# Kernel tuning notes

Measured on AMD Instinct MI355X. Metric: run time of the kernel, lower is better.

## Reference

```python
import jax, jax.numpy as jnp
import numpy as np

B, E, S = 8, 128, 4096


def setup_inputs() -> dict:
    key = jax.random.key(0)
    ks = jax.random.split(key, 7)
    sc = 1.0 / np.sqrt(E)
    return {
        "x": jax.random.normal(ks[0], (B, E, S), dtype=jnp.float32),
        "Wq": jax.random.normal(ks[1], (E, E), dtype=jnp.float32) * sc,
        "bq": jax.random.normal(ks[2], (E,), dtype=jnp.float32) * 0.01,
        "Wk": jax.random.normal(ks[3], (E, E), dtype=jnp.float32) * sc,
        "bk": jax.random.normal(ks[4], (E,), dtype=jnp.float32) * 0.01,
        "Wv": jax.random.normal(ks[5], (E, E), dtype=jnp.float32) * sc,
        "bv": jax.random.normal(ks[6], (E,), dtype=jnp.float32) * 0.01,
    }


def reference(x, Wq, bq, Wk, bk, Wv, bv):
    # x: [B, E, S]; Conv1d(k=1) == per-position linear over channels.
    # Project then move to [B, S, E] (matches .permute(0, 2, 1)).
    Q = jnp.einsum('bes,fe->bsf', x, Wq) + bq  # [B, S, E]
    K = jnp.einsum('bes,fe->bsf', x, Wk) + bk
    V = jnp.einsum('bes,fe->bsf', x, Wv) + bv
    scale = jnp.sqrt(jnp.asarray(float(x.shape[1]), dtype=jnp.float32))
    attn = jnp.einsum('bqe,bke->bqk', Q, K) / scale  # [B, S, S]
    attn = jax.nn.softmax(attn, axis=2)
    out = jnp.einsum('bqk,bke->bqe', attn, V)  # [B, S, E]
    return out.transpose(0, 2, 1)  # [B, E, S]
```

## Files before the change

kernel.cpp:

```cpp
#include <hip/hip_runtime.h>
#include <math.h>

#define NB 8
#define NE 128
#define NS 4096
#define CSCALE 0.12751743f

typedef short s8v __attribute__((ext_vector_type(8)));
typedef float f4v __attribute__((ext_vector_type(4)));
typedef float f16v __attribute__((ext_vector_type(16)));
typedef unsigned int u32;
typedef unsigned int u2v __attribute__((ext_vector_type(2)));
typedef __attribute__((address_space(1))) const u32* gp1_t;
typedef __attribute__((address_space(3))) u32* lp3_t;

__device__ __forceinline__ ushort f2bf(float f) {
  union { float f; unsigned u; } v; v.f = f;
  unsigned r = v.u + 0x7fffu + ((v.u >> 16) & 1u);
  return (ushort)(r >> 16);
}
__device__ __forceinline__ float bf2f(ushort h) {
  union { unsigned u; float f; } v; v.u = ((unsigned)h) << 16; return v.f;
}
__device__ __forceinline__ void gload_lds16(const void* g, void* l) {
  __builtin_amdgcn_global_load_lds((gp1_t)g, (lp3_t)l, 16, 0, 0);
}
__device__ __forceinline__ u32 cvtpk(float lo, float hi) {
  u32 r;
  asm("v_cvt_pk_bf16_f32 %0, %1, %2" : "=v"(r) : "v"(lo), "v"(hi));
  return r;
}
__device__ __forceinline__ void split8(const float* __restrict__ p, float scale,
                                       s8v& hi, s8v& lo) {
  union { s8v v; ushort u[8]; } H, L;
  #pragma unroll
  for (int i = 0; i < 8; ++i) {
    float v = p[i] * scale;
    ushort h = f2bf(v);
    H.u[i] = h;
    L.u[i] = f2bf(v - bf2f(h));
  }
  hi = H.v; lo = L.v;
}

__global__ __launch_bounds__(256, 2) void proj_gemm(
    const float* __restrict__ x,
    const float* __restrict__ Wq, const float* __restrict__ bq,
    const float* __restrict__ Wk, const float* __restrict__ bk,
    const float* __restrict__ Wv, const float* __restrict__ bv,
    ushort* __restrict__ Qn, ushort* __restrict__ Kn, ushort* __restrict__ Vt)
{
  const int tid = threadIdx.x;
  const int wv = tid >> 6, lane = tid & 63;
  const int g = lane >> 4, c = lane & 15;
  const int bid = blockIdx.x;
  const int b = bid & 7;
  const int s0 = (bid >> 3) * 64;
  const float* xb = x + (size_t)b * NE * NS;

  __shared__ __align__(16) ushort xh[64][136], xl[64][136];

  {
    const int ss = tid & 63, cq = tid >> 6;
    #pragma unroll
    for (int p = 0; p < 4; ++p) {
      const int ch = p * 4 + cq;
      union { s8v v; ushort u[8]; } H, L;
      #pragma unroll
      for (int i = 0; i < 8; ++i) {
        float v = xb[(size_t)(ch * 8 + i) * NS + s0 + ss];
        ushort hi = f2bf(v);
        H.u[i] = hi;
        L.u[i] = f2bf(v - bf2f(hi));
      }
      *(s8v*)&xh[ss][ch * 8] = H.v;
      *(s8v*)&xl[ss][ch * 8] = L.v;
    }
  }
  __syncthreads();

  f4v aq[2][4], ak[2][4], av[2][4];
  #pragma unroll
  for (int i = 0; i < 2; ++i)
    #pragma unroll
    for (int j = 0; j < 4; ++j) {
      aq[i][j] = (f4v){0.f,0.f,0.f,0.f};
      ak[i][j] = (f4v){0.f,0.f,0.f,0.f};
      av[i][j] = (f4v){0.f,0.f,0.f,0.f};
    }

  #pragma unroll
  for (int ks = 0; ks < 4; ++ks) {
    s8v xbh[4], xbl[4];
    #pragma unroll
    for (int st = 0; st < 4; ++st) {
      xbh[st] = *(const s8v*)&xh[st * 16 + c][ks * 32 + g * 8];
      xbl[st] = *(const s8v*)&xl[st * 16 + c][ks * 32 + g * 8];
    }
    #pragma unroll
    for (int ftl = 0; ftl < 2; ++ftl) {
      const int f0 = (wv * 2 + ftl) * 16;
      const size_t wo = (size_t)(f0 + c) * NE + ks * 32 + g * 8;
      s8v qh, ql, kh, kl, vh, vl;
      split8(Wq + wo, CSCALE, qh, ql);
      split8(Wk + wo, 1.0f,   kh, kl);
      split8(Wv + wo, 1.0f,   vh, vl);
      #pragma unroll
      for (int st = 0; st < 4; ++st) {
        aq[ftl][st] = __builtin_amdgcn_mfma_f32_16x16x32_bf16(xbh[st], qh, aq[ftl][st], 0, 0, 0);
        aq[ftl][st] = __builtin_amdgcn_mfma_f32_16x16x32_bf16(xbl[st], qh, aq[ftl][st], 0, 0, 0);
        aq[ftl][st] = __builtin_amdgcn_mfma_f32_16x16x32_bf16(xbh[st], ql, aq[ftl][st], 0, 0, 0);
        av[ftl][st] = __builtin_amdgcn_mfma_f32_16x16x32_bf16(vh, xbh[st], av[ftl][st], 0, 0, 0);
        av[ftl][st] = __builtin_amdgcn_mfma_f32_16x16x32_bf16(vh, xbl[st], av[ftl][st], 0, 0, 0);
        av[ftl][st] = __builtin_amdgcn_mfma_f32_16x16x32_bf16(vl, xbh[st], av[ftl][st], 0, 0, 0);
        ak[ftl][st] = __builtin_amdgcn_mfma_f32_16x16x32_bf16(xbh[st], kh, ak[ftl][st], 0, 0, 0);
        ak[ftl][st] = __builtin_amdgcn_mfma_f32_16x16x32_bf16(xbl[st], kh, ak[ftl][st], 0, 0, 0);
        ak[ftl][st] = __builtin_amdgcn_mfma_f32_16x16x32_bf16(xbh[st], kl, ak[ftl][st], 0, 0, 0);
      }
    }
  }

  ushort* Qnb = Qn + (size_t)b * NS * NE;
  ushort* Knb = Kn + (size_t)b * NS * NE;
  ushort* Vtb = Vt + (size_t)b * NE * NS;
  #pragma unroll
  for (int ftl = 0; ftl < 2; ++ftl) {
    const int f0 = (wv * 2 + ftl) * 16;
    #pragma unroll
    for (int r = 0; r < 4; ++r) {
      const int f = f0 + 4 * g + r;
      const float bvv = bv[f];
      #pragma unroll
      for (int st = 0; st < 4; ++st)
        Vtb[(size_t)f * NS + s0 + st * 16 + c] = f2bf(av[ftl][st][r] + bvv);
    }
    const float bqv = bq[f0 + c] * CSCALE;
    const float bkv = bk[f0 + c];
    #pragma unroll
    for (int st = 0; st < 4; ++st)
      #pragma unroll
      for (int r = 0; r < 4; ++r) {
        const size_t ro = (size_t)(s0 + st * 16 + 4 * g + r) * NE + f0 + c;
        Qnb[ro] = f2bf(aq[ftl][st][r] + bqv);
        Knb[ro] = f2bf(ak[ftl][st][r] + bkv);
      }
  }
}

__global__ __launch_bounds__(512, 2) void attn_kernel(
    const ushort* __restrict__ Qn, const ushort* __restrict__ Kn,
    const ushort* __restrict__ Vt, float* __restrict__ out)
{
  const int tid = threadIdx.x;
  const int w = tid >> 6, lane = tid & 63;
  const int h = lane >> 5, q5 = lane & 31;
  const int slice = w >> 2;
  const int sub = w & 3;
  const int bid = blockIdx.x;
  const int b = bid & 7;
  const int qw = (bid >> 3) * 128 + sub * 32;

  const ushort* Qb = Qn + (size_t)b * NS * NE;
  const char*   Kb = (const char*)(Kn + (size_t)b * NS * NE);
  const char*   Vb = (const char*)(Vt + (size_t)b * NE * NS);

  __shared__ __align__(16) char lds[131072];
  __shared__ float lx[2][4][32];

  auto Kbuf = [&](int bf) -> char* { return lds + slice * 65536 + bf * 32768; };
  auto Vbuf = [&](int bf) -> char* { return Kbuf(bf) + 16384; };

  s8v qf[8];
  #pragma unroll
  for (int dc = 0; dc < 8; ++dc)
    qf[dc] = *(const s8v*)(Qb + (size_t)(qw + q5) * NE + dc * 16 + h * 8);

  auto stage = [&](int bf, int t) {
    const int kt = slice * 32 + t;
    if (sub < 2) {
      const char* Ksrc = Kb + (size_t)kt * (64 * 256);
      char* dst = Kbuf(bf);
      const int base = sub * 8192;
      #pragma unroll
      for (int p = 0; p < 8; ++p) {
        const int off = base + p * 1024;
        const int lo = off + lane * 16;
        const int row = lo >> 8;
        gload_lds16(Ksrc + (lo ^ ((row & 15) << 4)), dst + off);
      }
    } else {
      char* dst = Vbuf(bf);
      const int base = (sub - 2) * 8192;
      #pragma unroll
      for (int p = 0; p < 8; ++p) {
        const int off = base + p * 1024;
        const int lo = off + lane * 16;
        const int row = lo >> 7;
        const int inner = (lo & 127) ^ ((row & 7) << 4);
        gload_lds16(Vb + (size_t)row * (NS * 2) + kt * 128 + inner, dst + off);
      }
    }
  };

  auto expfrag8 = [&](float a0, float a1, float a2, float a3,
                      float a4, float a5, float a6, float a7, float& l) -> s8v {
    float p0 = __builtin_amdgcn_exp2f(a0), p1 = __builtin_amdgcn_exp2f(a1);
    float p2 = __builtin_amdgcn_exp2f(a2), p3 = __builtin_amdgcn_exp2f(a3);
    float p4 = __builtin_amdgcn_exp2f(a4), p5 = __builtin_amdgcn_exp2f(a5);
    float p6 = __builtin_amdgcn_exp2f(a6), p7 = __builtin_amdgcn_exp2f(a7);
    l += ((p0 + p1) + (p2 + p3)) + ((p4 + p5) + (p6 + p7));
    u32 A = cvtpk(p0, p1);
    u32 B = cvtpk(p4, p5);
    u32 C = cvtpk(p2, p3);
    u32 D = cvtpk(p6, p7);
    u2v rAB = __builtin_amdgcn_permlane32_swap(A, B, false, false);
    u2v rCD = __builtin_amdgcn_permlane32_swap(C, D, false, false);
    union { s8v v; u32 wd[4]; } P;
    P.wd[0] = rAB[0]; P.wd[1] = rCD[0]; P.wd[2] = rAB[1]; P.wd[3] = rCD[1];
    return P.v;
  };

  f16v o[4];
  #pragma unroll
  for (int dt = 0; dt < 4; ++dt)
    o[dt] = (f16v){0,0,0,0,0,0,0,0,0,0,0,0,0,0,0,0};
  float lsum = 0.f;

  stage(0, 0);
  asm volatile("s_waitcnt vmcnt(0)" ::: "memory");
  __builtin_amdgcn_sched_barrier(0);
  __builtin_amdgcn_s_barrier();

  #pragma unroll 1
  for (int t = 0; t < 32; ++t) {
    const int cur = t & 1;
    if (t + 1 < 32) stage(cur ^ 1, t + 1);
    const char* bK = Kbuf(cur);
    const char* bV = Vbuf(cur);

    f16v s0 = (f16v){0,0,0,0,0,0,0,0,0,0,0,0,0,0,0,0};
    f16v s1 = (f16v){0,0,0,0,0,0,0,0,0,0,0,0,0,0,0,0};
    __builtin_amdgcn_s_setprio(1);
    #pragma unroll
    for (int dc = 0; dc < 8; ++dc) {
      s8v kf0 = *(const s8v*)(bK + (q5) * 256      + ((dc * 32 + h * 16) ^ ((q5 & 15) << 4)));
      s8v kf1 = *(const s8v*)(bK + (32 + q5) * 256 + ((dc * 32 + h * 16) ^ ((q5 & 15) << 4)));
      s0 = __builtin_amdgcn_mfma_f32_32x32x16_bf16(kf0, qf[dc], s0, 0, 0, 0);
      s1 = __builtin_amdgcn_mfma_f32_32x32x16_bf16(kf1, qf[dc], s1, 0, 0, 0);
    }
    __builtin_amdgcn_s_setprio(0);

    #pragma unroll
    for (int ks = 0; ks < 4; ++ks) {
      s8v P;
      if (ks == 0)      P = expfrag8(s0[0], s0[1], s0[2], s0[3], s0[4], s0[5], s0[6], s0[7], lsum);
      else if (ks == 1) P = expfrag8(s0[8], s0[9], s0[10], s0[11], s0[12], s0[13], s0[14], s0[15], lsum);
      else if (ks == 2) P = expfrag8(s1[0], s1[1], s1[2], s1[3], s1[4], s1[5], s1[6], s1[7], lsum);
      else              P = expfrag8(s1[8], s1[9], s1[10], s1[11], s1[12], s1[13], s1[14], s1[15], lsum);
      __builtin_amdgcn_s_setprio(1);
      #pragma unroll
      for (int dt = 0; dt < 4; ++dt) {
        s8v vf = *(const s8v*)(bV + (dt * 32 + q5) * 128 +
                               ((ks * 32 + h * 16) ^ ((q5 & 7) << 4)));
        o[dt] = __builtin_amdgcn_mfma_f32_32x32x16_bf16(vf, P, o[dt], 0, 0, 0);
      }
      __builtin_amdgcn_s_setprio(0);
    }

    asm volatile("s_waitcnt lgkmcnt(0)" ::: "memory");
    __builtin_amdgcn_sched_barrier(0);
    asm volatile("s_waitcnt vmcnt(0)" ::: "memory");
    __builtin_amdgcn_sched_barrier(0);
    __builtin_amdgcn_s_barrier();
  }

  lsum += __shfl_xor(lsum, 32);
  if (h == 0) lx[slice][sub][q5] = lsum;
  float* cb = (float*)lds;
  __syncthreads();
  if (slice == 1) {
    #pragma unroll
    for (int dt = 0; dt < 4; ++dt)
      #pragma unroll
      for (int r = 0; r < 16; ++r) {
        const int e = dt * 32 + (r & 3) + 8 * (r >> 2) + 4 * h;
        cb[sub * 4096 + e * 32 + q5] = o[dt][r];
      }
  }
  __syncthreads();
  if (slice == 0) {
    const float rinv = 1.0f / (lx[0][sub][q5] + lx[1][sub][q5]);
    float* ob = out + (size_t)b * NE * NS;
    #pragma unroll
    for (int dt = 0; dt < 4; ++dt)
      #pragma unroll
      for (int r = 0; r < 16; ++r) {
        const int e = dt * 32 + (r & 3) + 8 * (r >> 2) + 4 * h;
        ob[(size_t)e * NS + qw + q5] =
            (o[dt][r] + cb[sub * 4096 + e * 32 + q5]) * rinv;
      }
  }
}

extern "C" void kernel_launch(void* const* d_in, const int* in_sizes, int n_in,
                              void* d_out, int out_size, void* d_ws, size_t ws_size,
                              hipStream_t stream) {
  (void)in_sizes; (void)n_in; (void)out_size; (void)ws_size;
  const float* x  = (const float*)d_in[0];
  const float* Wq = (const float*)d_in[1];
  const float* bq = (const float*)d_in[2];
  const float* Wk = (const float*)d_in[3];
  const float* bk = (const float*)d_in[4];
  const float* Wv = (const float*)d_in[5];
  const float* bv = (const float*)d_in[6];
  float* out = (float*)d_out;

  ushort* Qn = (ushort*)d_ws;
  ushort* Kn = Qn + (size_t)NB * NS * NE;
  ushort* Vt = Kn + (size_t)NB * NS * NE;

  proj_gemm<<<dim3(NS / 64 * NB), 256, 0, stream>>>(x, Wq, bq, Wk, bk, Wv, bv, Qn, Kn, Vt);
  attn_kernel<<<dim3(NS / 128 * NB), 512, 0, stream>>>(Qn, Kn, Vt, out);
}
```

Before: 101.9 us.

## Software-pipeline QK and PV across tiles with lagged V staging

Measured after the change: 100.7 us. No clear change (-1.2%).

```diff
diff --git a/kernel.cpp b/kernel.cpp
--- a/kernel.cpp
+++ b/kernel.cpp
@@ -175,9 +175,9 @@
   for (int dc = 0; dc < 8; ++dc)
     qf[dc] = *(const s8v*)(Qb + (size_t)(qw + q5) * NE + dc * 16 + h * 8);
 
-  auto stage = [&](int bf, int t) {
-    const int kt = slice * 32 + t;
+  auto stageK = [&](int bf, int t) {
     if (sub < 2) {
+      const int kt = slice * 32 + t;
       const char* Ksrc = Kb + (size_t)kt * (64 * 256);
       char* dst = Kbuf(bf);
       const int base = sub * 8192;
@@ -188,16 +188,21 @@
         const int row = lo >> 8;
         gload_lds16(Ksrc + (lo ^ ((row & 15) << 4)), dst + off);
       }
-    } else {
+    }
+  };
+  auto stageV = [&](int bf, int t) {
+    if (sub >= 2) {
+      const int kt = slice * 32 + t;
       char* dst = Vbuf(bf);
       const int base = (sub - 2) * 8192;
       #pragma unroll
       for (int p = 0; p < 8; ++p) {
         const int off = base + p * 1024;
         const int lo = off + lane * 16;
-        const int row = lo >> 7;
-        const int inner = (lo & 127) ^ ((row & 7) << 4);
-        gload_lds16(Vb + (size_t)row * (NS * 2) + kt * 128 + inner, dst + off);
+        const int row = lo >> 8;
+        const int inner = (lo & 255) ^ ((row & 15) << 4);
+        const int d = row + (inner >> 7) * 64;
+        gload_lds16(Vb + (size_t)d * (NS * 2) + kt * 128 + (inner & 127), dst + off);
       }
     }
   };
@@ -220,58 +225,75 @@
     return P.v;
   };
 
+  auto pv16 = [&](const char* bV, int ks, s8v P, f16v* o) {
+    __builtin_amdgcn_s_setprio(1);
+    #pragma unroll
+    for (int dt = 0; dt < 4; ++dt) {
+      const int d = dt * 32 + q5;
+      const int row = d & 63;
+      const int col = ((dt >> 1) * 128 + ks * 32 + h * 16) ^ ((row & 15) << 4);
+      s8v vf = *(const s8v*)(bV + row * 256 + col);
+      o[dt] = __builtin_amdgcn_mfma_f32_32x32x16_bf16(vf, P, o[dt], 0, 0, 0);
+    }
+    __builtin_amdgcn_s_setprio(0);
+  };
+
   f16v o[4];
   #pragma unroll
   for (int dt = 0; dt < 4; ++dt)
     o[dt] = (f16v){0,0,0,0,0,0,0,0,0,0,0,0,0,0,0,0};
   float lsum = 0.f;
-
-  stage(0, 0);
+  s8v P0 = (s8v){0,0,0,0,0,0,0,0}, P1 = P0, P2 = P0, P3 = P0;
+
+  stageK(0, 0);
   asm volatile("s_waitcnt vmcnt(0)" ::: "memory");
   __builtin_amdgcn_sched_barrier(0);
   __builtin_amdgcn_s_barrier();
 
   #pragma unroll 1
   for (int t = 0; t < 32; ++t) {
-    const int cur = t & 1;
-    if (t + 1 < 32) stage(cur ^ 1, t + 1);
-    const char* bK = Kbuf(cur);
-    const char* bV = Vbuf(cur);
-
-    f16v s0 = (f16v){0,0,0,0,0,0,0,0,0,0,0,0,0,0,0,0};
-    f16v s1 = (f16v){0,0,0,0,0,0,0,0,0,0,0,0,0,0,0,0};
+    if (t + 1 < 32) stageK((t + 1) & 1, t + 1);
+    stageV(t & 1, t);
+
+    const char* bK = Kbuf(t & 1);
+    f16v s0v = (f16v){0,0,0,0,0,0,0,0,0,0,0,0,0,0,0,0};
+    f16v s1v = (f16v){0,0,0,0,0,0,0,0,0,0,0,0,0,0,0,0};
     __builtin_amdgcn_s_setprio(1);
     #pragma unroll
     for (int dc = 0; dc < 8; ++dc) {
       s8v kf0 = *(const s8v*)(bK + (q5) * 256      + ((dc * 32 + h * 16) ^ ((q5 & 15) << 4)));
       s8v kf1 = *(const s8v*)(bK + (32 + q5) * 256 + ((dc * 32 + h * 16) ^ ((q5 & 15) << 4)));
-      s0 = __builtin_amdgcn_mfma_f32_32x32x16_bf16(kf0, qf[dc], s0, 0, 0, 0);
-      s1 = __builtin_amdgcn_mfma_f32_32x32x16_bf16(kf1, qf[dc], s1, 0, 0, 0);
+      s0v = __builtin_amdgcn_mfma_f32_32x32x16_bf16(kf0, qf[dc], s0v, 0, 0, 0);
+      s1v = __builtin_amdgcn_mfma_f32_32x32x16_bf16(kf1, qf[dc], s1v, 0, 0, 0);
     }
     __builtin_amdgcn_s_setprio(0);
 
-    #pragma unroll
-    for (int ks = 0; ks < 4; ++ks) {
-      s8v P;
-      if (ks == 0)      P = expfrag8(s0[0], s0[1], s0[2], s0[3], s0[4], s0[5], s0[6], s0[7], lsum);
-      else if (ks == 1) P = expfrag8(s0[8], s0[9], s0[10], s0[11], s0[12], s0[13], s0[14], s0[15], lsum);
-      else if (ks == 2) P = expfrag8(s1[0], s1[1], s1[2], s1[3], s1[4], s1[5], s1[6], s1[7], lsum);
-      else              P = expfrag8(s1[8], s1[9], s1[10], s1[11], s1[12], s1[13], s1[14], s1[15], lsum);
-      __builtin_amdgcn_s_setprio(1);
-      #pragma unroll
-      for (int dt = 0; dt < 4; ++dt) {
-        s8v vf = *(const s8v*)(bV + (dt * 32 + q5) * 128 +
-                               ((ks * 32 + h * 16) ^ ((q5 & 7) << 4)));
-        o[dt] = __builtin_amdgcn_mfma_f32_32x32x16_bf16(vf, P, o[dt], 0, 0, 0);
-      }
-      __builtin_amdgcn_s_setprio(0);
-    }
+    if (t > 0) {
+      const char* bV = Vbuf((t - 1) & 1);
+      pv16(bV, 0, P0, o);
+      pv16(bV, 1, P1, o);
+      pv16(bV, 2, P2, o);
+      pv16(bV, 3, P3, o);
+    }
+
+    P0 = expfrag8(s0v[0], s0v[1], s0v[2], s0v[3], s0v[4], s0v[5], s0v[6], s0v[7], lsum);
+    P1 = expfrag8(s0v[8], s0v[9], s0v[10], s0v[11], s0v[12], s0v[13], s0v[14], s0v[15], lsum);
+    P2 = expfrag8(s1v[0], s1v[1], s1v[2], s1v[3], s1v[4], s1v[5], s1v[6], s1v[7], lsum);
+    P3 = expfrag8(s1v[8], s1v[9], s1v[10], s1v[11], s1v[12], s1v[13], s1v[14], s1v[15], lsum);
 
     asm volatile("s_waitcnt lgkmcnt(0)" ::: "memory");
     __builtin_amdgcn_sched_barrier(0);
     asm volatile("s_waitcnt vmcnt(0)" ::: "memory");
     __builtin_amdgcn_sched_barrier(0);
     __builtin_amdgcn_s_barrier();
+  }
+
+  {
+    const char* bV = Vbuf(31 & 1);
+    pv16(bV, 0, P0, o);
+    pv16(bV, 1, P1, o);
+    pv16(bV, 2, P2, o);
+    pv16(bV, 3, P3, o);
   }
 
   lsum += __shfl_xor(lsum, 32);
```
